# Performance work log

Hardware: AMD Instinct MI355X
Metric: run time of the kernel (lower is better)

Reference implementation:

```python
import jax, jax.numpy as jnp
import numpy as np

DIM = 1024
NUM_HEADS = 16
NUM_KV_HEADS = 2
HEAD_DIM = DIM // NUM_HEADS          # 64
REPEATS = NUM_HEADS // NUM_KV_HEADS  # 8
WINDOW = 256
HALF = WINDOW // 2                   # 128
BATCH, SEQ = 2, 2048


def setup_inputs() -> dict:
    key = jax.random.key(0)
    ks = jax.random.split(key, 9)
    sc = 1.0 / np.sqrt(DIM)
    return {
        "x":  jax.random.normal(ks[0], (BATCH, SEQ, DIM), jnp.float32),
        "Wq": jax.random.normal(ks[1], (DIM, NUM_HEADS * HEAD_DIM), jnp.float32) * sc,
        "bq": jax.random.normal(ks[2], (NUM_HEADS * HEAD_DIM,), jnp.float32) * 0.01,
        "Wk": jax.random.normal(ks[3], (DIM, NUM_KV_HEADS * HEAD_DIM), jnp.float32) * sc,
        "bk": jax.random.normal(ks[4], (NUM_KV_HEADS * HEAD_DIM,), jnp.float32) * 0.01,
        "Wv": jax.random.normal(ks[5], (DIM, NUM_KV_HEADS * HEAD_DIM), jnp.float32) * sc,
        "bv": jax.random.normal(ks[6], (NUM_KV_HEADS * HEAD_DIM,), jnp.float32) * 0.01,
        "Wo": jax.random.normal(ks[7], (DIM, DIM), jnp.float32) * sc,
        "bo": jax.random.normal(ks[8], (DIM,), jnp.float32) * 0.01,
    }


def reference(x, Wq, bq, Wk, bk, Wv, bv, Wo, bo):
    # Training-path GQA sliding-window attention (faithful to the torch module):
    #  - K/V zero-padded by HALF on each side of the sequence; window of size
    #    WINDOW centered on each query position (unfold with step 1).
    #  - NOTE (faithful): the original code builds mask = tril(ones)[-1], which is
    #    an all-ones row, so masked_fill is a no-op -> NO causal mask inside the
    #    window; padded positions contribute score 0 (not -inf) to the softmax.
    #  - NOTE (faithful): the training path does NOT scale scores by 1/sqrt(d).
    b, s, _ = x.shape
    q = (x @ Wq + bq).reshape(b, s, NUM_HEADS, HEAD_DIM).transpose(0, 2, 1, 3)      # [b,H,s,d]
    k = (x @ Wk + bk).reshape(b, s, NUM_KV_HEADS, HEAD_DIM).transpose(0, 2, 1, 3)   # [b,G,s,d]
    v = (x @ Wv + bv).reshape(b, s, NUM_KV_HEADS, HEAD_DIM).transpose(0, 2, 1, 3)

    kp = jnp.pad(k, ((0, 0), (0, 0), (HALF, HALF), (0, 0)))  # [b,G,s+W,d]
    vp = jnp.pad(v, ((0, 0), (0, 0), (HALF, HALF), (0, 0)))

    # window gather indices: window i covers padded positions [i, i+W)
    idx = jnp.arange(s)[:, None] + jnp.arange(WINDOW)[None, :]  # [s,W]
    k_win = kp[:, :, idx]  # [b,G,s,W,d]  (gather at kv-head granularity, not H)
    v_win = vp[:, :, idx]

    # group query heads by kv head: head h -> kv group h // REPEATS
    qg = q.reshape(b, NUM_KV_HEADS, REPEATS, s, HEAD_DIM)        # [b,G,r,s,d]
    scores = jnp.einsum('bgrsd,bgswd->bgrsw', qg, k_win)         # no scaling (faithful)
    probs = jax.nn.softmax(scores, axis=-1)
    out = jnp.einsum('bgrsw,bgswd->bgrsd', probs, v_win)         # [b,G,r,s,d]

    out = out.reshape(b, NUM_HEADS, s, HEAD_DIM).transpose(0, 2, 1, 3).reshape(b, s, DIM)
    return out @ Wo + bo
```

## Files before the change

kernel.cpp:

```cpp
#include <hip/hip_runtime.h>
#include <hip/hip_fp16.h>

typedef _Float16 h16;
typedef __attribute__((ext_vector_type(4))) _Float16 h16x4;
typedef __attribute__((ext_vector_type(8))) _Float16 h16x8;
typedef __attribute__((ext_vector_type(4))) float f32x4;

#define DIM   1024
#define SEQ   2048
#define NKV   2
#define HD    64
#define HALFW 128
#define NQKV  1280
#define SPAD  2304
#define KPS   (SPAD*HD)
#define KSTG  288
#define VSTR  312
#define PSTR  296
#define LOG2E 1.4426950408889634f

__global__ void preprocess_kernel(const float* __restrict__ x,
                                  const float* __restrict__ bq,
                                  const float* __restrict__ bk,
                                  const float* __restrict__ bv,
                                  const float* __restrict__ Wq,
                                  const float* __restrict__ Wk,
                                  const float* __restrict__ Wv,
                                  const float* __restrict__ Wo,
                                  h16* __restrict__ xh, float* __restrict__ bqkv,
                                  h16* __restrict__ wqkvt, h16* __restrict__ wot,
                                  h16* __restrict__ kpad, h16* __restrict__ vtpad)
{
    __shared__ float tile[32][33];
    const int tid = threadIdx.x;
    const int blk = blockIdx.x;
    if (blk < 2048) {
        int i = blk * 256 + tid;
        size_t base = (size_t)i * 8;
        float4 a = *(const float4*)(x + base);
        float4 b = *(const float4*)(x + base + 4);
        h16x8 o = { (h16)a.x,(h16)a.y,(h16)a.z,(h16)a.w,
                    (h16)b.x,(h16)b.y,(h16)b.z,(h16)b.w };
        *(h16x8*)(xh + base) = o;
        if (i < NQKV) {
            float v = (i < DIM) ? bq[i] * LOG2E
                                : (i < DIM+128 ? bk[i-DIM] : bv[i-DIM-128]);
            bqkv[i] = v;
        }
        return;
    }
    if (blk >= 4352) {
        int idx = (blk - 4352) * 256 + tid;
        h16x8 z8 = {};
        h16* dstb = (idx < 16384) ? kpad : vtpad;
        int i2 = idx & 16383;
        int bg = i2 >> 12, j = i2 & 4095;
        if (j < 2048) {
            size_t off;
            if (idx < 16384) {
                off = (j < 1024) ? (size_t)j*8 : (size_t)2176*HD + (size_t)(j-1024)*8;
            } else {
                int d = j >> 5, r = j & 31;
                off = (size_t)d*SPAD + ((r & 16) ? 2176 : 0) + (size_t)(r & 15)*8;
            }
            *(h16x8*)(dstb + (size_t)bg*KPS + off) = z8;
        }
        return;
    }
    const int tx = tid & 31, ty = tid >> 5;
    if (blk < 2048 + 1280) {
        int bid = blk - 2048;
        int n0 = (bid % 40) * 32, k0 = (bid / 40) * 32;
        const float* src; int ldn, noff; float scl;
        if (n0 < DIM)          { src = Wq; ldn = DIM; noff = n0; scl = LOG2E; }
        else if (n0 < DIM+128) { src = Wk; ldn = 128; noff = n0 - DIM; scl = 1.f; }
        else                   { src = Wv; ldn = 128; noff = n0 - DIM - 128; scl = 1.f; }
#pragma unroll
        for (int i = 0; i < 4; ++i)
            tile[ty + 8*i][tx] = src[(size_t)(k0 + ty + 8*i)*ldn + noff + tx] * scl;
        __syncthreads();
#pragma unroll
        for (int i = 0; i < 4; ++i)
            wqkvt[(size_t)(n0 + ty + 8*i)*DIM + k0 + tx] = (h16)tile[tx][ty + 8*i];
    } else {
        int bid = blk - 3328;
        int n0 = (bid % 32) * 32, k0 = (bid / 32) * 32;
#pragma unroll
        for (int i = 0; i < 4; ++i)
            tile[ty + 8*i][tx] = Wo[(size_t)(k0 + ty + 8*i)*DIM + n0 + tx];
        __syncthreads();
#pragma unroll
        for (int i = 0; i < 4; ++i)
            wot[(size_t)(n0 + ty + 8*i)*DIM + k0 + tx] = (h16)tile[tx][ty + 8*i];
    }
}

template<int MODE>
__global__ __launch_bounds__(256, 2)
void gemm_kernel(const h16* __restrict__ A, const h16* __restrict__ Bt,
                 const float* __restrict__ bias,
                 h16* __restrict__ qo, h16* __restrict__ ko, h16* __restrict__ vo,
                 float* __restrict__ co, int K, int nx)
{
    __shared__ __align__(16) h16 lds[2][2][128*64];
    const int nwg = gridDim.x, bid = blockIdx.x;
    const int wg = (bid & 7) * (nwg >> 3) + (bid >> 3);
    const int m0 = (wg / nx) * 128, n0 = (wg % nx) * 128;
    const int tid = threadIdx.x, lane = tid & 63, wid = tid >> 6;
    const int wr = wid >> 1, wc = wid & 1;
    f32x4 acc[4][4] = {};

    auto stage = [&](int buf, int kk) {
#pragma unroll
        for (int i = 0; i < 4; ++i) {
            int slot = i*256 + tid;
            int row = slot >> 3;
            int scol = ((slot & 7) ^ (row & 7)) * 8;
            __builtin_amdgcn_global_load_lds(
                (const __attribute__((address_space(1))) void*)(A + (size_t)(m0 + row)*K + kk + scol),
                (__attribute__((address_space(3))) void*)(&lds[buf][0][slot*8]), 16, 0, 0);
        }
#pragma unroll
        for (int i = 0; i < 4; ++i) {
            int slot = i*256 + tid;
            int row = slot >> 3;
            int scol = ((slot & 7) ^ (row & 7)) * 8;
            __builtin_amdgcn_global_load_lds(
                (const __attribute__((address_space(1))) void*)(Bt + (size_t)(n0 + row)*K + kk + scol),
                (__attribute__((address_space(3))) void*)(&lds[buf][1][slot*8]), 16, 0, 0);
        }
    };
    auto compute = [&](int buf) {
#pragma unroll
        for (int k2 = 0; k2 < 2; ++k2) {
            h16x8 a[4], b[4];
#pragma unroll
            for (int mi = 0; mi < 4; ++mi) {
                int row = wr*64 + mi*16 + (lane & 15);
                int cc = (k2*4 + (lane >> 4)) ^ (row & 7);
                a[mi] = *(const h16x8*)(&lds[buf][0][row*64 + cc*8]);
            }
#pragma unroll
            for (int ni = 0; ni < 4; ++ni) {
                int row = wc*64 + ni*16 + (lane & 15);
                int cc = (k2*4 + (lane >> 4)) ^ (row & 7);
                b[ni] = *(const h16x8*)(&lds[buf][1][row*64 + cc*8]);
            }
#pragma unroll
            for (int mi = 0; mi < 4; ++mi)
#pragma unroll
                for (int ni = 0; ni < 4; ++ni)
                    acc[mi][ni] = __builtin_amdgcn_mfma_f32_16x16x32_f16(a[mi], b[ni], acc[mi][ni], 0, 0, 0);
        }
    };

    const int ns = K >> 6;
    stage(0, 0);
    int cur = 0;
    for (int i = 0; i < ns; ++i) {
        if (i < ns-1) {
            stage(cur ^ 1, (i+1) << 6);
            asm volatile("s_waitcnt vmcnt(8)" ::: "memory");
        } else {
            asm volatile("s_waitcnt vmcnt(0)" ::: "memory");
        }
        __builtin_amdgcn_s_barrier();
        __builtin_amdgcn_sched_barrier(0);
        compute(cur);
        if (i < ns-1) {
            __builtin_amdgcn_s_barrier();
            __builtin_amdgcn_sched_barrier(0);
        }
        cur ^= 1;
    }

    if (MODE == 0 && n0 == DIM + 128) {
        __syncthreads();
        h16* T = &lds[0][0][0];
#pragma unroll
        for (int ni = 0; ni < 4; ++ni) {
            int nrel = wc*64 + ni*16 + (lane & 15);
            float bv = bias[n0 + nrel];
#pragma unroll
            for (int mi = 0; mi < 4; ++mi) {
                int mrel = wr*64 + mi*16 + (lane >> 4)*4;
#pragma unroll
                for (int r = 0; r < 4; ++r)
                    T[nrel*136 + mrel + r] = (h16)(acc[mi][ni][r] + bv);
            }
        }
        __syncthreads();
        const int bi2 = m0 >> 11, sbase = m0 & 2047;
#pragma unroll
        for (int i = 0; i < 8; ++i) {
            int slot = i*256 + tid;
            int nrel = slot >> 4, cc = slot & 15;
            int g = nrel >> 6, d = nrel & 63;
            h16x8 val = *(const h16x8*)(T + nrel*136 + cc*8);
            *(h16x8*)(vo + ((size_t)(bi2*NKV + g))*KPS + (size_t)d*SPAD
                      + HALFW + sbase + cc*8) = val;
        }
        return;
    }

#pragma unroll
    for (int ni = 0; ni < 4; ++ni) {
        int n = n0 + wc*64 + ni*16 + (lane & 15);
        float bv = bias[n];
#pragma unroll
        for (int mi = 0; mi < 4; ++mi) {
            int mb = m0 + wr*64 + mi*16 + (lane >> 4)*4;
#pragma unroll
            for (int r = 0; r < 4; ++r) {
                int m = mb + r;
                float v = acc[mi][ni][r] + bv;
                if (MODE == 1) {
                    co[(size_t)m*DIM + n] = v;
                } else {
                    h16 hv = (h16)v;
                    if (n < DIM) {
                        qo[(size_t)m*DIM + n] = hv;
                    } else {
                        int nn = n - DIM;
                        int bi2 = m >> 11, s = m & 2047;
                        int g = nn >> 6, d = nn & 63;
                        ko[((size_t)(bi2*NKV + g)*SPAD + s + HALFW)*HD + d] = hv;
                    }
                }
            }
        }
    }
}

__global__ __launch_bounds__(512)
void attn_kernel(const h16* __restrict__ qb, const h16* __restrict__ kpad,
                 const h16* __restrict__ vtpad, h16* __restrict__ ob)
{
    extern __shared__ char smem[];
    h16* Ks  = (h16*)smem;
    h16* Vts = (h16*)(smem + 36864);
    h16* Ps  = (h16*)(smem + 76800);
    const int tid = threadIdx.x, lane = tid & 63, wid = tid >> 6;
    const int qt = blockIdx.x, g = blockIdx.y, bi = blockIdx.z;
    const int s0 = qt * 32;
    const h16* Kbase = kpad  + (size_t)(bi*NKV + g)*KPS + (size_t)s0*HD;
    const h16* Vbase = vtpad + (size_t)(bi*NKV + g)*KPS + s0;

    for (int slot = tid; slot < KSTG*8; slot += 512) {
        int row = slot >> 3, cc = slot & 7;
        h16x8 val = *(const h16x8*)(Kbase + (size_t)row*HD + cc*8);
        *(h16x8*)(Ks + row*64 + ((cc ^ (row & 7)) * 8)) = val;
    }
    for (int slot = tid; slot < 64*38; slot += 512) {
        int row = slot / 38, cc = slot - row*38;
        h16x8 val = *(const h16x8*)(Vbase + (size_t)row*SPAD + cc*8);
        *(h16x8*)(Vts + row*VSTR + cc*8) = val;
    }
    h16* P = Ps + wid * 16 * PSTR;
    for (int i = lane; i < 256; i += 64)
        P[(i >> 4)*PSTR + 272 + (i & 15)] = (h16)0;
    __syncthreads();

    const int h = g*8 + wid;
    const int colbase = lane & 15;
    const int rowbase = (lane >> 4) * 4;
    const int kg = rowbase;

    for (int strip = 0; strip < 2; ++strip) {
        const int ss0 = s0 + strip*16;
        h16x8 aq[2];
#pragma unroll
        for (int c = 0; c < 2; ++c)
            aq[c] = *(const h16x8*)(qb + ((size_t)(bi*SEQ + ss0 + colbase))*DIM
                                    + h*HD + c*32 + (lane >> 4)*8);

        f32x4 sc[17];
        __builtin_amdgcn_s_setprio(1);
#pragma unroll
        for (int t = 0; t < 17; ++t) {
            f32x4 z = {0.f,0.f,0.f,0.f};
#pragma unroll
            for (int c = 0; c < 2; ++c) {
                int key = strip*16 + t*16 + colbase;
                h16x8 kf = *(const h16x8*)(Ks + key*64 + (((c*4 + (lane >> 4)) ^ (key & 7)) * 8));
                z = __builtin_amdgcn_mfma_f32_16x16x32_f16(kf, aq[c], z, 0, 0, 0);
            }
            sc[t] = z;
        }
        __builtin_amdgcn_s_setprio(0);

        float mx = -1e30f;
#pragma unroll
        for (int r = 0; r < 4; ++r) {
            float v0  = (kg + r >= colbase) ? sc[0][r]  : -1e30f;
            float v16 = (kg + r <  colbase) ? sc[16][r] : -1e30f;
            sc[0][r] = v0; sc[16][r] = v16;
            mx = fmaxf(mx, fmaxf(v0, v16));
        }
#pragma unroll
        for (int t = 1; t < 16; t += 3) {
#pragma unroll
            for (int r = 0; r < 4; ++r) {
                float a = sc[t][r];
                float b = (t+1 < 16) ? sc[t+1][r] : -1e30f;
                float c2 = (t+2 < 16) ? sc[t+2][r] : -1e30f;
                mx = fmaxf(mx, fmaxf(fmaxf(a, b), c2));
            }
        }
        mx = fmaxf(mx, __shfl_xor(mx, 16));
        mx = fmaxf(mx, __shfl_xor(mx, 32));
        float sum = 0.f;
#pragma unroll
        for (int t = 0; t < 17; ++t)
#pragma unroll
            for (int r = 0; r < 4; ++r) {
                float p = exp2f(sc[t][r] - mx);
                sc[t][r] = p;
                sum += p;
            }
        sum += __shfl_xor(sum, 16);
        sum += __shfl_xor(sum, 32);
        float inv = 1.0f / sum;

#pragma unroll
        for (int t = 0; t < 17; ++t) {
            h16x4 pk = { (h16)sc[t][0], (h16)sc[t][1],
                         (h16)sc[t][2], (h16)sc[t][3] };
            *(h16x4*)(P + colbase*PSTR + t*16 + kg) = pk;
        }

        f32x4 ao[4] = {};
        __builtin_amdgcn_s_setprio(1);
#pragma unroll
        for (int c = 0; c < 9; ++c) {
            h16x8 pa = *(const h16x8*)(P + colbase*PSTR + c*32 + (lane >> 4)*8);
            int vcol = strip*16 + c*32 + (lane >> 4)*8;
#pragma unroll
            for (int t2 = 0; t2 < 4; ++t2) {
                h16x8 vb = *(const h16x8*)(Vts + (t2*16 + colbase)*VSTR + vcol);
                ao[t2] = __builtin_amdgcn_mfma_f32_16x16x32_f16(pa, vb, ao[t2], 0, 0, 0);
            }
        }
        __builtin_amdgcn_s_setprio(0);

#pragma unroll
        for (int r = 0; r < 4; ++r) {
            int qrow = rowbase + r;
            float iq = __shfl(inv, qrow);
            size_t rowoff = ((size_t)(bi*SEQ + ss0 + qrow))*DIM + h*HD;
#pragma unroll
            for (int t2 = 0; t2 < 4; ++t2)
                ob[rowoff + t2*16 + colbase] = (h16)(ao[t2][r] * iq);
        }
    }
}

extern "C" void kernel_launch(void* const* d_in, const int* in_sizes, int n_in,
                              void* d_out, int out_size, void* d_ws, size_t ws_size,
                              hipStream_t stream)
{
    const float* x  = (const float*)d_in[0];
    const float* Wq = (const float*)d_in[1];
    const float* bq = (const float*)d_in[2];
    const float* Wk = (const float*)d_in[3];
    const float* bk = (const float*)d_in[4];
    const float* Wv = (const float*)d_in[5];
    const float* bv = (const float*)d_in[6];
    const float* Wo = (const float*)d_in[7];
    const float* bo = (const float*)d_in[8];
    float* out = (float*)d_out;
    char* ws = (char*)d_ws;

    h16*   xh    = (h16*)(ws);
    h16*   wqkvt = (h16*)(ws + 8388608);
    h16*   wot   = (h16*)(ws + 11010048);
    float* bqkv  = (float*)(ws + 13107200);
    h16*   q_b   = (h16*)(ws + 13112320);
    h16*   k_pad = (h16*)(ws + 21500928);
    h16*   vt_pad= (h16*)(ws + 22680576);
    h16*   att_b = (h16*)(ws + 23860224);

    preprocess_kernel<<<4480, 256, 0, stream>>>(x, bq, bk, bv, Wq, Wk, Wv, Wo,
                                                xh, bqkv, wqkvt, wot, k_pad, vt_pad);
    gemm_kernel<0><<<320, 256, 0, stream>>>(xh, wqkvt, bqkv,
                                            q_b, k_pad, vt_pad, nullptr, DIM, 10);
    hipFuncSetAttribute((const void*)attn_kernel,
                        hipFuncAttributeMaxDynamicSharedMemorySize, 152576);
    attn_kernel<<<dim3(64, 2, 2), 512, 152576, stream>>>(q_b, k_pad, vt_pad, att_b);
    gemm_kernel<1><<<256, 256, 0, stream>>>(att_b, wot, bo,
                                            nullptr, nullptr, nullptr, out, DIM, 8);
}
```

Baseline: 64.26 us.

## Fuse fp32-to-fp16 conversion of x into the QKV GEMM A-tile loads

The separate pass that converted x to fp16 in the preprocess kernel is removed. The QKV GEMM now reads fp32 x straight into registers, converts it, and writes fp16 into LDS, with the global loads software-pipelined across iterations. This drops an 8 MB fp16 write plus its re-read and shrinks the preprocess grid. In exchange, the GEMM reads twice the A bytes in fp32, uses more registers, and replaces the direct global-to-LDS DMA with a register round-trip that may hurt occupancy and overlap.

```diff
diff --git a/kernel.cpp b/kernel.cpp
--- a/kernel.cpp
+++ b/kernel.cpp
@@ -19,38 +19,27 @@
 #define PSTR  296
 #define LOG2E 1.4426950408889634f
 
-__global__ void preprocess_kernel(const float* __restrict__ x,
-                                  const float* __restrict__ bq,
+__global__ void preprocess_kernel(const float* __restrict__ bq,
                                   const float* __restrict__ bk,
                                   const float* __restrict__ bv,
                                   const float* __restrict__ Wq,
                                   const float* __restrict__ Wk,
                                   const float* __restrict__ Wv,
                                   const float* __restrict__ Wo,
-                                  h16* __restrict__ xh, float* __restrict__ bqkv,
+                                  float* __restrict__ bqkv,
                                   h16* __restrict__ wqkvt, h16* __restrict__ wot,
                                   h16* __restrict__ kpad, h16* __restrict__ vtpad)
 {
     __shared__ float tile[32][33];
     const int tid = threadIdx.x;
     const int blk = blockIdx.x;
-    if (blk < 2048) {
-        int i = blk * 256 + tid;
-        size_t base = (size_t)i * 8;
-        float4 a = *(const float4*)(x + base);
-        float4 b = *(const float4*)(x + base + 4);
-        h16x8 o = { (h16)a.x,(h16)a.y,(h16)a.z,(h16)a.w,
-                    (h16)b.x,(h16)b.y,(h16)b.z,(h16)b.w };
-        *(h16x8*)(xh + base) = o;
-        if (i < NQKV) {
-            float v = (i < DIM) ? bq[i] * LOG2E
-                                : (i < DIM+128 ? bk[i-DIM] : bv[i-DIM-128]);
-            bqkv[i] = v;
-        }
-        return;
-    }
-    if (blk >= 4352) {
-        int idx = (blk - 4352) * 256 + tid;
+    if (blk >= 2304) {
+        int idx = (blk - 2304) * 256 + tid;
+        if (idx < NQKV) {
+            float v = (idx < DIM) ? bq[idx] * LOG2E
+                                  : (idx < DIM+128 ? bk[idx-DIM] : bv[idx-DIM-128]);
+            bqkv[idx] = v;
+        }
         h16x8 z8 = {};
         h16* dstb = (idx < 16384) ? kpad : vtpad;
         int i2 = idx & 16383;
@@ -68,8 +57,8 @@
         return;
     }
     const int tx = tid & 31, ty = tid >> 5;
-    if (blk < 2048 + 1280) {
-        int bid = blk - 2048;
+    if (blk < 1280) {
+        int bid = blk;
         int n0 = (bid % 40) * 32, k0 = (bid / 40) * 32;
         const float* src; int ldn, noff; float scl;
         if (n0 < DIM)          { src = Wq; ldn = DIM; noff = n0; scl = LOG2E; }
@@ -83,7 +72,7 @@
         for (int i = 0; i < 4; ++i)
             wqkvt[(size_t)(n0 + ty + 8*i)*DIM + k0 + tx] = (h16)tile[tx][ty + 8*i];
     } else {
-        int bid = blk - 3328;
+        int bid = blk - 1280;
         int n0 = (bid % 32) * 32, k0 = (bid / 32) * 32;
 #pragma unroll
         for (int i = 0; i < 4; ++i)
@@ -97,7 +86,7 @@
 
 template<int MODE>
 __global__ __launch_bounds__(256, 2)
-void gemm_kernel(const h16* __restrict__ A, const h16* __restrict__ Bt,
+void gemm_kernel(const void* __restrict__ Ap, const h16* __restrict__ Bt,
                  const float* __restrict__ bias,
                  h16* __restrict__ qo, h16* __restrict__ ko, h16* __restrict__ vo,
                  float* __restrict__ co, int K, int nx)
@@ -109,17 +98,10 @@
     const int tid = threadIdx.x, lane = tid & 63, wid = tid >> 6;
     const int wr = wid >> 1, wc = wid & 1;
     f32x4 acc[4][4] = {};
-
-    auto stage = [&](int buf, int kk) {
-#pragma unroll
-        for (int i = 0; i < 4; ++i) {
-            int slot = i*256 + tid;
-            int row = slot >> 3;
-            int scol = ((slot & 7) ^ (row & 7)) * 8;
-            __builtin_amdgcn_global_load_lds(
-                (const __attribute__((address_space(1))) void*)(A + (size_t)(m0 + row)*K + kk + scol),
-                (__attribute__((address_space(3))) void*)(&lds[buf][0][slot*8]), 16, 0, 0);
-        }
+    const float* Af = (const float*)Ap;
+    const h16*   Ah = (const h16*)Ap;
+
+    auto loadB = [&](int buf, int kk) {
 #pragma unroll
         for (int i = 0; i < 4; ++i) {
             int slot = i*256 + tid;
@@ -155,23 +137,74 @@
     };
 
     const int ns = K >> 6;
-    stage(0, 0);
-    int cur = 0;
-    for (int i = 0; i < ns; ++i) {
-        if (i < ns-1) {
-            stage(cur ^ 1, (i+1) << 6);
-            asm volatile("s_waitcnt vmcnt(8)" ::: "memory");
-        } else {
-            asm volatile("s_waitcnt vmcnt(0)" ::: "memory");
-        }
-        __builtin_amdgcn_s_barrier();
-        __builtin_amdgcn_sched_barrier(0);
-        compute(cur);
-        if (i < ns-1) {
+    if constexpr (MODE == 0) {
+        float4 ra[8];
+        auto loadA = [&](int kk) {
+#pragma unroll
+            for (int i = 0; i < 4; ++i) {
+                int slot = i*256 + tid;
+                int row = slot >> 3;
+                int scol = ((slot & 7) ^ (row & 7)) * 8;
+                const float* src = Af + (size_t)(m0 + row)*K + kk + scol;
+                ra[2*i]   = *(const float4*)(src);
+                ra[2*i+1] = *(const float4*)(src + 4);
+            }
+        };
+        auto writeA = [&](int buf) {
+#pragma unroll
+            for (int i = 0; i < 4; ++i) {
+                int slot = i*256 + tid;
+                float4 a = ra[2*i], b = ra[2*i+1];
+                h16x8 o = { (h16)a.x,(h16)a.y,(h16)a.z,(h16)a.w,
+                            (h16)b.x,(h16)b.y,(h16)b.z,(h16)b.w };
+                *(h16x8*)(&lds[buf][0][slot*8]) = o;
+            }
+        };
+        loadA(0); loadB(0, 0);
+        asm volatile("s_waitcnt vmcnt(4)" ::: "memory");
+        writeA(0);
+        __syncthreads();
+        int cur = 0;
+        for (int i = 0; i < ns; ++i) {
+            if (i < ns-1) { loadA((i+1) << 6); loadB(cur ^ 1, (i+1) << 6); }
+            compute(cur);
+            if (i < ns-1) {
+                asm volatile("s_waitcnt vmcnt(4)" ::: "memory");
+                writeA(cur ^ 1);
+                __syncthreads();
+            }
+            cur ^= 1;
+        }
+    } else {
+        auto loadA16 = [&](int buf, int kk) {
+#pragma unroll
+            for (int i = 0; i < 4; ++i) {
+                int slot = i*256 + tid;
+                int row = slot >> 3;
+                int scol = ((slot & 7) ^ (row & 7)) * 8;
+                __builtin_amdgcn_global_load_lds(
+                    (const __attribute__((address_space(1))) void*)(Ah + (size_t)(m0 + row)*K + kk + scol),
+                    (__attribute__((address_space(3))) void*)(&lds[buf][0][slot*8]), 16, 0, 0);
+            }
+        };
+        loadA16(0, 0); loadB(0, 0);
+        int cur = 0;
+        for (int i = 0; i < ns; ++i) {
+            if (i < ns-1) {
+                loadA16(cur ^ 1, (i+1) << 6); loadB(cur ^ 1, (i+1) << 6);
+                asm volatile("s_waitcnt vmcnt(8)" ::: "memory");
+            } else {
+                asm volatile("s_waitcnt vmcnt(0)" ::: "memory");
+            }
             __builtin_amdgcn_s_barrier();
             __builtin_amdgcn_sched_barrier(0);
-        }
-        cur ^= 1;
+            compute(cur);
+            if (i < ns-1) {
+                __builtin_amdgcn_s_barrier();
+                __builtin_amdgcn_sched_barrier(0);
+            }
+            cur ^= 1;
+        }
     }
 
     if (MODE == 0 && n0 == DIM + 128) {
@@ -371,7 +404,6 @@
     float* out = (float*)d_out;
     char* ws = (char*)d_ws;
 
-    h16*   xh    = (h16*)(ws);
     h16*   wqkvt = (h16*)(ws + 8388608);
     h16*   wot   = (h16*)(ws + 11010048);
     float* bqkv  = (float*)(ws + 13107200);
@@ -380,13 +412,13 @@
     h16*   vt_pad= (h16*)(ws + 22680576);
     h16*   att_b = (h16*)(ws + 23860224);
 
-    preprocess_kernel<<<4480, 256, 0, stream>>>(x, bq, bk, bv, Wq, Wk, Wv, Wo,
-                                                xh, bqkv, wqkvt, wot, k_pad, vt_pad);
-    gemm_kernel<0><<<320, 256, 0, stream>>>(xh, wqkvt, bqkv,
+    preprocess_kernel<<<2432, 256, 0, stream>>>(bq, bk, bv, Wq, Wk, Wv, Wo,
+                                                bqkv, wqkvt, wot, k_pad, vt_pad);
+    gemm_kernel<0><<<320, 256, 0, stream>>>((const void*)x, wqkvt, bqkv,
                                             q_b, k_pad, vt_pad, nullptr, DIM, 10);
     hipFuncSetAttribute((const void*)attn_kernel,
                         hipFuncAttributeMaxDynamicSharedMemorySize, 152576);
     attn_kernel<<<dim3(64, 2, 2), 512, 152576, stream>>>(q_b, k_pad, vt_pad, att_b);
-    gemm_kernel<1><<<256, 256, 0, stream>>>(att_b, wot, bo,
+    gemm_kernel<1><<<256, 256, 0, stream>>>((const void*)att_b, wot, bo,
                                             nullptr, nullptr, nullptr, out, DIM, 8);
 }
```

Result: slower. 65.83 us (+2.5%).
